# Optimization experiments

Measured on AMD Instinct MI355X. Metric: run time of the kernel, lower is better.

Reference implementation:

```python
import jax, jax.numpy as jnp
import numpy as np

B, T, F, U = 32768, 7, 36, 256

def setup_inputs() -> dict:
    key = jax.random.key(0)
    ks = jax.random.split(key, 5)
    x = jax.random.normal(ks[0], (B, T, F), dtype=jnp.float32)
    h0 = jax.random.normal(ks[1], (B, U), dtype=jnp.float32)
    c0 = jax.random.normal(ks[2], (B, U), dtype=jnp.float32)
    Wk = jax.random.normal(ks[3], (F, 4 * U), dtype=jnp.float32) * 0.1
    Wr = jax.random.normal(ks[4], (U, 4 * U), dtype=jnp.float32) * 0.05
    b = jnp.zeros((4 * U,), dtype=jnp.float32)
    return {"x": x, "h0": h0, "c0": c0, "Wk": Wk, "Wr": Wr, "b": b}

def reference(x, h0, c0, Wk, Wr, b):
    # Precompute input projection for all 7 steps: [B,T,4U]
    zx = jnp.einsum('btf,fg->btg', x, Wk) + b
    zx_t = jnp.transpose(zx, (1, 0, 2))  # time-major [T,B,4U]

    def step(carry, z_in):
        h, c = carry
        z = z_in + h @ Wr  # [B,4U]
        i, f, g, o = jnp.split(z, 4, axis=-1)  # Keras gate order i,f,g,o
        i = jax.nn.sigmoid(i)
        f = jax.nn.sigmoid(f)
        g = jnp.tanh(g)
        o = jax.nn.sigmoid(o)
        c_new = f * c + i * g
        h_new = o * jnp.tanh(c_new)
        return (h_new, c_new), h_new

    (_, _), hs = jax.lax.scan(step, (h0, c0), zx_t)
    return jnp.transpose(hs, (1, 0, 2))  # [B,T,U] (return_sequences=True)
```

## Files before the change

kernel.cpp:

```cpp
#include <hip/hip_runtime.h>

typedef _Float16 half8 __attribute__((ext_vector_type(8)));
typedef float f32x4 __attribute__((ext_vector_type(4)));

#define B_TOTAL 32768
#define T 7
#define F 36
#define U 256
#define G4 1024
#define BM 64
#define KC 10
#define KPACK 32
#define H_STRIDE 264
#define XS 72

__global__ __launch_bounds__(1024) void pack_w(const float* __restrict__ Wr,
                                               const float* __restrict__ Wk,
                                               _Float16* __restrict__ Wq) {
    const int kc   = blockIdx.x >> 2;
    const int kin0 = (blockIdx.x & 3) * 8;
    const int n    = threadIdx.x;
    _Float16* dst = Wq + ((size_t)kc * G4 + n) * KPACK + kin0;
    #pragma unroll
    for (int j = 0; j < 8; ++j) {
        int k = kc * KPACK + kin0 + j;
        float v = 0.f;
        if (k < U)          v = Wr[(size_t)k * G4 + n];
        else if (k < U + F) v = Wk[(size_t)(k - U) * G4 + n];
        dst[j] = (_Float16)v;
    }
}

__device__ __forceinline__ float fast_sigmoid(float x) {
    return __builtin_amdgcn_rcpf(1.f + __expf(-x));
}
__device__ __forceinline__ float fast_tanh(float x) {
    return 1.f - 2.f * __builtin_amdgcn_rcpf(1.f + __expf(2.f * x));
}

__global__ __launch_bounds__(1024) void lstm_kernel(
    const float* __restrict__ x,
    const float* __restrict__ h0,
    const float* __restrict__ c0,
    const _Float16* __restrict__ Wq,
    const float* __restrict__ bias_g,
    float* __restrict__ out)
{
    __shared__ __align__(16) _Float16 hbuf[2][BM * H_STRIDE];
    __shared__ __align__(16) _Float16 xs[T * BM * XS];

    const int tid  = threadIdx.x;
    const int lane = tid & 63;
    const int w    = tid >> 6;
    const int l15  = lane & 15;
    const int q    = lane >> 4;
    const int u0   = w * 16;
    const int b0   = blockIdx.x * BM;

    {
        half8 z = {};
        for (int i = tid * 8; i < T * BM * XS; i += 1024 * 8)
            *(half8*)&xs[i] = z;
    }
    __syncthreads();

    for (int i = tid; i < BM * U; i += 1024) {
        int m = i >> 8, u = i & 255;
        hbuf[0][m * H_STRIDE + u] = (_Float16)h0[(size_t)b0 * U + i];
    }
    for (int i = tid; i < BM * (T * F); i += 1024) {
        int row = i / (T * F);
        int rem = i - row * (T * F);
        int t   = rem / F;
        int f   = rem - t * F;
        xs[(t * BM + row) * XS + f] = (_Float16)x[(size_t)(b0 + row) * (T * F) + rem];
    }
    float c[16];
    #pragma unroll
    for (int mt = 0; mt < 4; ++mt)
        #pragma unroll
        for (int r = 0; r < 4; ++r) {
            int row = mt * 16 + q * 4 + r;
            c[mt * 4 + r] = c0[(size_t)(b0 + row) * U + u0 + l15];
        }
    float bv[4];
    #pragma unroll
    for (int g = 0; g < 4; ++g) bv[g] = bias_g[g * U + u0 + l15];

    __syncthreads();

    int cur = 0;
    #pragma unroll 1
    for (int t = 0; t < T; ++t) {
        f32x4 acc[4][4];
        #pragma unroll
        for (int mt = 0; mt < 4; ++mt)
            #pragma unroll
            for (int g = 0; g < 4; ++g)
                acc[mt][g] = (f32x4){bv[g], bv[g], bv[g], bv[g]};

        #pragma unroll 2
        for (int kc = 0; kc < KC; ++kc) {
            half8 bf[4];
            #pragma unroll
            for (int g = 0; g < 4; ++g) {
                size_t off = ((size_t)kc * G4 + g * U + u0 + l15) * KPACK + q * 8;
                bf[g] = *(const half8*)(Wq + off);
            }
            #pragma unroll
            for (int mt = 0; mt < 4; ++mt) {
                half8 af;
                if (kc < 8)
                    af = *(const half8*)&hbuf[cur][(mt * 16 + l15) * H_STRIDE + kc * 32 + q * 8];
                else
                    af = *(const half8*)&xs[(t * BM + mt * 16 + l15) * XS + (kc - 8) * 32 + q * 8];
                #pragma unroll
                for (int g = 0; g < 4; ++g)
                    acc[mt][g] = __builtin_amdgcn_mfma_f32_16x16x32_f16(af, bf[g], acc[mt][g], 0, 0, 0);
            }
        }

        const int nxt = cur ^ 1;
        #pragma unroll
        for (int mt = 0; mt < 4; ++mt)
            #pragma unroll
            for (int r = 0; r < 4; ++r) {
                float zi = acc[mt][0][r];
                float zf = acc[mt][1][r];
                float zg = acc[mt][2][r];
                float zo = acc[mt][3][r];
                float ig = fast_sigmoid(zi);
                float fg = fast_sigmoid(zf);
                float gg = fast_tanh(zg);
                float og = fast_sigmoid(zo);
                float cn = fg * c[mt * 4 + r] + ig * gg;
                c[mt * 4 + r] = cn;
                float hv = og * fast_tanh(cn);
                int row = mt * 16 + q * 4 + r;
                hbuf[nxt][row * H_STRIDE + u0 + l15] = (_Float16)hv;
            }

        __syncthreads();

        #pragma unroll
        for (int rb = 0; rb < 2; ++rb) {
            int j   = tid + rb * 1024;
            int row = j >> 5;
            int uo  = (j & 31) * 8;
            half8 hv = *(const half8*)&hbuf[nxt][row * H_STRIDE + uo];
            f32x4 lo = { (float)hv[0], (float)hv[1], (float)hv[2], (float)hv[3] };
            f32x4 hi = { (float)hv[4], (float)hv[5], (float)hv[6], (float)hv[7] };
            float* dst = out + ((size_t)(b0 + row) * T + t) * U + uo;
            *(f32x4*)dst       = lo;
            *(f32x4*)(dst + 4) = hi;
        }

        cur = nxt;
    }
}

extern "C" void kernel_launch(void* const* d_in, const int* in_sizes, int n_in,
                              void* d_out, int out_size, void* d_ws, size_t ws_size,
                              hipStream_t stream) {
    const float* x  = (const float*)d_in[0];
    const float* h0 = (const float*)d_in[1];
    const float* c0 = (const float*)d_in[2];
    const float* Wk = (const float*)d_in[3];
    const float* Wr = (const float*)d_in[4];
    const float* b  = (const float*)d_in[5];
    float* out = (float*)d_out;

    _Float16* Wq = (_Float16*)d_ws;

    pack_w<<<KC * 4, 1024, 0, stream>>>(Wr, Wk, Wq);
    lstm_kernel<<<B_TOTAL / BM, 1024, 0, stream>>>(x, h0, c0, Wq, b, out);
}
```

Measured before the change: 486.2 us.

## Precompute next step's input projection before barrier and repack weights per wave

```diff
diff --git a/kernel.cpp b/kernel.cpp
--- a/kernel.cpp
+++ b/kernel.cpp
@@ -13,6 +13,7 @@
 #define KPACK 32
 #define H_STRIDE 264
 #define XS 72
+#define WKC (16 * 4 * 16 * KPACK)
 
 __global__ __launch_bounds__(1024) void pack_w(const float* __restrict__ Wr,
                                                const float* __restrict__ Wk,
@@ -20,7 +21,10 @@
     const int kc   = blockIdx.x >> 2;
     const int kin0 = (blockIdx.x & 3) * 8;
     const int n    = threadIdx.x;
-    _Float16* dst = Wq + ((size_t)kc * G4 + n) * KPACK + kin0;
+    const int g    = n >> 8;
+    const int w    = (n >> 4) & 15;
+    const int l15  = n & 15;
+    _Float16* dst = Wq + ((size_t)((kc * 16 + w) * 4 + g) * 16 + l15) * KPACK + kin0;
     #pragma unroll
     for (int j = 0; j < 8; ++j) {
         int k = kc * KPACK + kin0 + j;
@@ -38,7 +42,7 @@
     return 1.f - 2.f * __builtin_amdgcn_rcpf(1.f + __expf(2.f * x));
 }
 
-__global__ __launch_bounds__(1024) void lstm_kernel(
+__global__ __launch_bounds__(1024, 4) void lstm_kernel(
     const float* __restrict__ x,
     const float* __restrict__ h0,
     const float* __restrict__ c0,
@@ -87,36 +91,53 @@
     #pragma unroll
     for (int g = 0; g < 4; ++g) bv[g] = bias_g[g * U + u0 + l15];
 
+    const _Float16* wp = Wq + ((size_t)(w * 4) * 16 + l15) * KPACK + q * 8;
+
     __syncthreads();
+
+    f32x4 acc[4][4];
+
+    {
+        #pragma unroll
+        for (int mt = 0; mt < 4; ++mt)
+            #pragma unroll
+            for (int g = 0; g < 4; ++g)
+                acc[mt][g] = (f32x4){bv[g], bv[g], bv[g], bv[g]};
+        const _Float16* xbase = &xs[(size_t)l15 * XS + q * 8];
+        #pragma unroll
+        for (int kx = 8; kx < 10; ++kx) {
+            half8 bf[4];
+            #pragma unroll
+            for (int g = 0; g < 4; ++g)
+                bf[g] = *(const half8*)(wp + (size_t)kx * WKC + g * (16 * KPACK));
+            #pragma unroll
+            for (int mt = 0; mt < 4; ++mt) {
+                half8 af = *(const half8*)(xbase + mt * 16 * XS + (kx - 8) * 32);
+                #pragma unroll
+                for (int g = 0; g < 4; ++g)
+                    acc[mt][g] = __builtin_amdgcn_mfma_f32_16x16x32_f16(af, bf[g], acc[mt][g], 0, 0, 0);
+            }
+        }
+    }
 
     int cur = 0;
     #pragma unroll 1
     for (int t = 0; t < T; ++t) {
-        f32x4 acc[4][4];
-        #pragma unroll
-        for (int mt = 0; mt < 4; ++mt)
-            #pragma unroll
-            for (int g = 0; g < 4; ++g)
-                acc[mt][g] = (f32x4){bv[g], bv[g], bv[g], bv[g]};
-
-        #pragma unroll 2
-        for (int kc = 0; kc < KC; ++kc) {
-            half8 bf[4];
-            #pragma unroll
-            for (int g = 0; g < 4; ++g) {
-                size_t off = ((size_t)kc * G4 + g * U + u0 + l15) * KPACK + q * 8;
-                bf[g] = *(const half8*)(Wq + off);
-            }
-            #pragma unroll
-            for (int mt = 0; mt < 4; ++mt) {
-                half8 af;
-                if (kc < 8)
-                    af = *(const half8*)&hbuf[cur][(mt * 16 + l15) * H_STRIDE + kc * 32 + q * 8];
-                else
-                    af = *(const half8*)&xs[(t * BM + mt * 16 + l15) * XS + (kc - 8) * 32 + q * 8];
-                #pragma unroll
-                for (int g = 0; g < 4; ++g)
-                    acc[mt][g] = __builtin_amdgcn_mfma_f32_16x16x32_f16(af, bf[g], acc[mt][g], 0, 0, 0);
+        {
+            const _Float16* hbase = &hbuf[cur][(size_t)l15 * H_STRIDE + q * 8];
+            #pragma unroll
+            for (int kc = 0; kc < 8; ++kc) {
+                half8 bf[4];
+                #pragma unroll
+                for (int g = 0; g < 4; ++g)
+                    bf[g] = *(const half8*)(wp + (size_t)kc * WKC + g * (16 * KPACK));
+                #pragma unroll
+                for (int mt = 0; mt < 4; ++mt) {
+                    half8 af = *(const half8*)(hbase + mt * 16 * H_STRIDE + kc * 32);
+                    #pragma unroll
+                    for (int g = 0; g < 4; ++g)
+                        acc[mt][g] = __builtin_amdgcn_mfma_f32_16x16x32_f16(af, bf[g], acc[mt][g], 0, 0, 0);
+                }
             }
         }
 
@@ -140,6 +161,29 @@
                 hbuf[nxt][row * H_STRIDE + u0 + l15] = (_Float16)hv;
             }
 
+        if (t + 1 < T) {
+            #pragma unroll
+            for (int mt = 0; mt < 4; ++mt)
+                #pragma unroll
+                for (int g = 0; g < 4; ++g)
+                    acc[mt][g] = (f32x4){bv[g], bv[g], bv[g], bv[g]};
+            const _Float16* xbase = &xs[((size_t)(t + 1) * BM + l15) * XS + q * 8];
+            #pragma unroll
+            for (int kx = 8; kx < 10; ++kx) {
+                half8 bf[4];
+                #pragma unroll
+                for (int g = 0; g < 4; ++g)
+                    bf[g] = *(const half8*)(wp + (size_t)kx * WKC + g * (16 * KPACK));
+                #pragma unroll
+                for (int mt = 0; mt < 4; ++mt) {
+                    half8 af = *(const half8*)(xbase + mt * 16 * XS + (kx - 8) * 32);
+                    #pragma unroll
+                    for (int g = 0; g < 4; ++g)
+                        acc[mt][g] = __builtin_amdgcn_mfma_f32_16x16x32_f16(af, bf[g], acc[mt][g], 0, 0, 0);
+                }
+            }
+        }
+
         __syncthreads();
 
         #pragma unroll
```

Result: slower. 702.2 us (+44.4%).
